# Kernel optimization log

Hardware: AMD Instinct MI355X
Metric: run time of the kernel (lower is better)

Reference implementation:

```python
import jax, jax.numpy as jnp
import numpy as np
from jax import lax

NUM_GROUPS = 16
POOL_KS = 2
CLAMP_MIN = 0.0
CLAMP_MAX = 1.0
EPS = 1e-5


def setup_inputs() -> dict:
    key = jax.random.key(0)
    k1, k2, k3, k4, k5 = jax.random.split(key, 5)
    B, Cin, H, W = 32, 64, 128, 128
    Cout, K = 128, 3
    x = jax.random.normal(k1, (B, Cin, H, W), dtype=jnp.float32)
    fan_in = Cin * K * K
    bound = 1.0 / np.sqrt(fan_in)
    conv_w = jax.random.uniform(k2, (Cout, Cin, K, K), jnp.float32, -bound, bound)
    conv_b = jax.random.uniform(k3, (Cout,), jnp.float32, -bound, bound)
    gn_w = jnp.ones((Cout,), jnp.float32)
    gn_b = jnp.zeros((Cout,), jnp.float32)
    scale = jnp.ones((Cout, 1, 1), jnp.float32)
    return {"x": x, "conv_w": conv_w, "conv_b": conv_b,
            "gn_w": gn_w, "gn_b": gn_b, "scale": scale}


def reference(x, conv_w, conv_b, gn_w, gn_b, scale):
    # Conv2d, stride=1, padding=0  -> (B, Cout, Ho, Wo)
    y = lax.conv_general_dilated(
        x, conv_w, window_strides=(1, 1), padding="VALID",
        dimension_numbers=("NCHW", "OIHW", "NCHW"))
    y = y + conv_b[None, :, None, None]
    B, C, H, W = y.shape
    G = NUM_GROUPS
    # GroupNorm (biased variance, as in torch)
    yg = y.reshape(B, G, C // G, H, W)
    mean = jnp.mean(yg, axis=(2, 3, 4), keepdims=True)
    var = jnp.mean(jnp.square(yg), axis=(2, 3, 4), keepdims=True) - jnp.square(mean)
    yn = (yg - mean) * lax.rsqrt(var + EPS)
    yn = yn.reshape(B, C, H, W) * gn_w[None, :, None, None] + gn_b[None, :, None, None]
    # per-channel scale
    yn = yn * scale[None, :, :, :]
    # MaxPool2d(kernel=POOL_KS, stride=POOL_KS), VALID
    pooled = lax.reduce_window(
        yn, -jnp.inf, lax.max,
        window_dimensions=(1, 1, POOL_KS, POOL_KS),
        window_strides=(1, 1, POOL_KS, POOL_KS),
        padding="VALID")
    return jnp.clip(pooled, CLAMP_MIN, CLAMP_MAX)
```

## Files before the change

kernel.cpp:

```cpp
#include <hip/hip_runtime.h>
#include <stdint.h>
#include <stddef.h>

#define HIN 128
#define WIN 128
#define CINC 64
#define COUTC 128
#define HO 126
#define WO 126
#define HP 63
#define WP 63
#define NB 32
#define NG 16

typedef __bf16 bf16x8 __attribute__((ext_vector_type(8)));
typedef float f32x16 __attribute__((ext_vector_type(16)));

#define AS1U(p) ((const __attribute__((address_space(1))) unsigned int*)(p))
#define AS3U(p) ((__attribute__((address_space(3))) unsigned int*)(p))

__device__ __forceinline__ unsigned int f2bf(float f) {
  unsigned int u = __float_as_uint(f);
  return (u + 0x7fffu + ((u >> 16) & 1u)) >> 16;
}

__global__ __launch_bounds__(256) void wtrans_k(const float* __restrict__ w,
                                                unsigned short* __restrict__ wt2) {
  int i = blockIdx.x * 256 + threadIdx.x;
  if (i >= 73728) return;
  int j = i & 7;
  int co = (i >> 3) & 127;
  int th = i >> 10;
  int half = th & 1, ks = (th >> 1) & 3, tap = th >> 3;
  int kh = tap / 3, kw = tap - 3 * kh;
  int cin = ks * 16 + half * 8 + j;
  float v = w[((co * CINC + cin) * 3 + kh) * 3 + kw];
  wt2[i] = (unsigned short)f2bf(v);
}

__global__ __launch_bounds__(256, 2) void conv_k(const float* __restrict__ x,
                                                 const unsigned short* __restrict__ wt2,
                                                 const float* __restrict__ conv_b,
                                                 float* __restrict__ out,
                                                 float* __restrict__ stats) {
  __shared__ __align__(16) unsigned int x_lds[18 * 18 * 32];
  __shared__ __align__(16) unsigned int aux_lds[8448];

  int t = threadIdx.x;
  int lane = t & 63, wave = t >> 6;
  int tw = blockIdx.x & 7, th = blockIdx.x >> 3;
  int b = blockIdx.y;
  int oh0 = th * 16, ow0 = tw * 16;

  const unsigned int* wg = (const unsigned int*)wt2;

#pragma unroll
  for (int j = 0; j < 4; ++j) {
    int dof = j * 1024 + wave * 256;
    __builtin_amdgcn_global_load_lds(AS1U(wg + dof + lane * 4), AS3U(&aux_lds[dof]),
                                     16, 0, 0);
  }

  const float* xb = x + (size_t)b * CINC * HIN * WIN;
  for (int i = t; i < 2880; i += 256) {
    int c4 = i % 5;
    int j = i / 5;
    int p = j & 31;
    int r = j >> 5;
    int gr = oh0 + r;
    int gc0 = ow0 + c4 * 4;
    float4 v0 = make_float4(0.f, 0.f, 0.f, 0.f);
    float4 v1 = v0;
    if (gr < HIN && gc0 < WIN) {
      const float* base = xb + ((size_t)(2 * p) * HIN + gr) * WIN + gc0;
      v0 = *(const float4*)base;
      v1 = *(const float4*)(base + HIN * WIN);
    }
    float e0[4] = {v0.x, v0.y, v0.z, v0.w};
    float e1[4] = {v1.x, v1.y, v1.z, v1.w};
#pragma unroll
    for (int cc = 0; cc < 4; ++cc) {
      int c = c4 * 4 + cc;
      if (c < 18) {
        unsigned int d = f2bf(e0[cc]) | (f2bf(e1[cc]) << 16);
        x_lds[(r * 18 + c) * 32 + (p ^ ((c & 7) << 2))] = d;
      }
    }
  }
  __syncthreads();

  int half = lane >> 5, m = lane & 31;
  f32x16 acc[2][4];
#pragma unroll
  for (int nt = 0; nt < 4; ++nt) {
    float bias = conv_b[nt * 32 + m];
#pragma unroll
    for (int mt = 0; mt < 2; ++mt)
#pragma unroll
      for (int r = 0; r < 16; ++r) acc[mt][nt][r] = bias;
  }

  int prb = wave * 4 + (m >> 4);
  int pcc = m & 15;

#pragma unroll
  for (int tap = 0; tap < 9; ++tap) {
    const int buf = tap & 1;
    if (tap < 8) {
#pragma unroll
      for (int j = 0; j < 4; ++j) {
        int dof = j * 1024 + wave * 256;
        __builtin_amdgcn_global_load_lds(
            AS1U(wg + (tap + 1) * 4096 + dof + lane * 4),
            AS3U(&aux_lds[(buf ^ 1) * 4096 + dof]), 16, 0, 0);
      }
    }
    const int kh = tap / 3, kw = tap - 3 * (tap / 3);
    int c = pcc + kw;
    int swz = (c & 7) << 2;
#pragma unroll
    for (int ks = 0; ks < 4; ++ks) {
      int ab = c * 32 + ((ks * 8 + half * 4) ^ swz);
      bf16x8 afr[2];
#pragma unroll
      for (int mt = 0; mt < 2; ++mt)
        afr[mt] = __builtin_bit_cast(
            bf16x8, *(const uint4*)&x_lds[(prb + mt * 2 + kh) * (18 * 32) + ab]);
      int wbase = buf * 4096 + ks * 1024 + half * 512 + m * 4;
#pragma unroll
      for (int nt = 0; nt < 4; ++nt) {
        bf16x8 bfr = __builtin_bit_cast(bf16x8, *(const uint4*)&aux_lds[wbase + nt * 128]);
#pragma unroll
        for (int mt = 0; mt < 2; ++mt)
          acc[mt][nt] = __builtin_amdgcn_mfma_f32_32x32x16_bf16(afr[mt], bfr,
                                                                acc[mt][nt], 0, 0, 0);
      }
    }
    __syncthreads();
  }

  float s[4] = {0.f, 0.f, 0.f, 0.f}, qs[4] = {0.f, 0.f, 0.f, 0.f};
#pragma unroll
  for (int nt = 0; nt < 4; ++nt) {
#pragma unroll
    for (int mt = 0; mt < 2; ++mt) {
#pragma unroll
      for (int reg = 0; reg < 16; ++reg) {
        int c16 = (reg & 3) + 4 * half + 8 * ((reg >> 2) & 1);
        int r8 = wave * 4 + mt * 2 + (reg >> 3);
        if ((oh0 + r8) < HO && (ow0 + c16) < WO) {
          float v = acc[mt][nt][reg];
          s[nt] += v;
          qs[nt] += v * v;
        }
      }
    }
  }
#pragma unroll
  for (int nt = 0; nt < 4; ++nt) {
    float sv = s[nt], qv = qs[nt];
    sv += __shfl_xor(sv, 32);
    qv += __shfl_xor(qv, 32);
    sv += __shfl_down(sv, 4, 8);
    qv += __shfl_down(qv, 4, 8);
    sv += __shfl_down(sv, 2, 8);
    qv += __shfl_down(qv, 2, 8);
    sv += __shfl_down(sv, 1, 8);
    qv += __shfl_down(qv, 1, 8);
    if (half == 0 && (m & 7) == 0) {
      int g = nt * 4 + (m >> 3);
      atomicAdd(&stats[(b * NG + g) * 2 + 0], sv);
      atomicAdd(&stats[(b * NG + g) * 2 + 1], qv);
    }
  }

#pragma unroll
  for (int nt = 0; nt < 4; ++nt) {
    int co = nt * 32 + m;
#pragma unroll
    for (int mt = 0; mt < 2; ++mt) {
      int oh2l = wave * 2 + mt;
#pragma unroll
      for (int i = 0; i < 4; ++i) {
        int r0 = 2 * i;
        int ow2l = (i & 1) + 2 * half + 4 * (i >> 1);
        float mx = fmaxf(fmaxf(acc[mt][nt][r0], acc[mt][nt][r0 + 1]),
                         fmaxf(acc[mt][nt][r0 + 8], acc[mt][nt][r0 + 9]));
        aux_lds[co * 66 + oh2l * 8 + ow2l] = __float_as_uint(mx);
      }
    }
  }
  __syncthreads();

#pragma unroll
  for (int i = 0; i < 4; ++i) {
    int row = t * 4 + i;
    int co = row >> 3, oh2l = row & 7;
    int oh2 = th * 8 + oh2l;
    if (oh2 < HP) {
      const uint2* src = (const uint2*)&aux_lds[co * 66 + oh2l * 8];
      uint2 d0 = src[0], d1 = src[1], d2 = src[2], d3 = src[3];
      unsigned int v[8] = {d0.x, d0.y, d1.x, d1.y, d2.x, d2.y, d3.x, d3.y};
      float* ob = out + ((size_t)(b * COUTC + co) * HP + oh2) * WP + tw * 8;
      int n = (tw == 7) ? 7 : 8;
#pragma unroll
      for (int e = 0; e < 8; ++e)
        if (e < n) ob[e] = __uint_as_float(v[e]);
    }
  }
}

__global__ __launch_bounds__(256) void fin_k(float* __restrict__ out,
                                             const float* __restrict__ stats,
                                             const float* __restrict__ gn_w,
                                             const float* __restrict__ gn_b,
                                             const float* __restrict__ scale) {
  const int total4 = NB * COUTC * HP * WP / 4;
  const float inv_cnt = 1.0f / (8.0f * HO * WO);
  int stride = gridDim.x * 256;
  for (int i4 = blockIdx.x * 256 + threadIdx.x; i4 < total4; i4 += stride) {
    float4 v = ((const float4*)out)[i4];
    float r[4] = {v.x, v.y, v.z, v.w};
    int idx0 = i4 * 4;
#pragma unroll
    for (int e = 0; e < 4; ++e) {
      int idx = idx0 + e;
      int bc = idx / (HP * WP);
      int c = bc & 127, b = bc >> 7;
      int g = c >> 3;
      float su = stats[(b * NG + g) * 2 + 0];
      float sq = stats[(b * NG + g) * 2 + 1];
      float mean = su * inv_cnt;
      float var = fmaxf(sq * inv_cnt - mean * mean, 0.f);
      float rstd = rsqrtf(var + 1e-5f);
      float A = rstd * gn_w[c] * scale[c];
      float B = (gn_b[c] - mean * rstd * gn_w[c]) * scale[c];
      r[e] = fminf(fmaxf(fmaf(r[e], A, B), 0.0f), 1.0f);
    }
    ((float4*)out)[i4] = make_float4(r[0], r[1], r[2], r[3]);
  }
}

extern "C" void kernel_launch(void* const* d_in, const int* in_sizes, int n_in,
                              void* d_out, int out_size, void* d_ws, size_t ws_size,
                              hipStream_t stream) {
  const float* x      = (const float*)d_in[0];
  const float* conv_w = (const float*)d_in[1];
  const float* conv_b = (const float*)d_in[2];
  const float* gn_w   = (const float*)d_in[3];
  const float* gn_b   = (const float*)d_in[4];
  const float* scale  = (const float*)d_in[5];
  float* out = (float*)d_out;

  float* stats        = (float*)d_ws;
  unsigned short* wt2 = (unsigned short*)((char*)d_ws + 4096);

  hipMemsetAsync(d_ws, 0, 4096, stream);
  wtrans_k<<<288, 256, 0, stream>>>(conv_w, wt2);

  conv_k<<<dim3(64, NB), 256, 0, stream>>>(x, wt2, conv_b, out, stats);

  fin_k<<<4096, 256, 0, stream>>>(out, stats, gn_w, gn_b, scale);
}
```

Before: 369.9 us.

## Load conv weights into registers, drop weight LDS, reorganize finalize per channel plane

The conv kernel no longer stages weights in LDS through global_load_lds. Each lane loads its B fragments straight from global memory into two register banks (wA/wB) that alternate across the nine taps, with the next tap's weights prefetched while the current tap's MFMAs run. Dropping the 33 KB aux buffer lets the pooled epilogue reuse x_lds, and the launch bound is raised to 3 blocks per CU. The finalize kernel now runs one block per (batch, channel) plane, computing the group-norm coefficients once instead of per element. The cost is 128 extra VGPRs for weight fragments, which may cause spills under the tighter launch bound, and duplicated global weight reads across waves.

```diff
diff --git a/kernel.cpp b/kernel.cpp
--- a/kernel.cpp
+++ b/kernel.cpp
@@ -15,9 +15,6 @@
 
 typedef __bf16 bf16x8 __attribute__((ext_vector_type(8)));
 typedef float f32x16 __attribute__((ext_vector_type(16)));
-
-#define AS1U(p) ((const __attribute__((address_space(1))) unsigned int*)(p))
-#define AS3U(p) ((__attribute__((address_space(3))) unsigned int*)(p))
 
 __device__ __forceinline__ unsigned int f2bf(float f) {
   unsigned int u = __float_as_uint(f);
@@ -38,28 +35,25 @@
   wt2[i] = (unsigned short)f2bf(v);
 }
 
-__global__ __launch_bounds__(256, 2) void conv_k(const float* __restrict__ x,
+__global__ __launch_bounds__(256, 3) void conv_k(const float* __restrict__ x,
                                                  const unsigned short* __restrict__ wt2,
                                                  const float* __restrict__ conv_b,
                                                  float* __restrict__ out,
                                                  float* __restrict__ stats) {
   __shared__ __align__(16) unsigned int x_lds[18 * 18 * 32];
-  __shared__ __align__(16) unsigned int aux_lds[8448];
 
   int t = threadIdx.x;
   int lane = t & 63, wave = t >> 6;
   int tw = blockIdx.x & 7, th = blockIdx.x >> 3;
   int b = blockIdx.y;
   int oh0 = th * 16, ow0 = tw * 16;
-
-  const unsigned int* wg = (const unsigned int*)wt2;
-
-#pragma unroll
-  for (int j = 0; j < 4; ++j) {
-    int dof = j * 1024 + wave * 256;
-    __builtin_amdgcn_global_load_lds(AS1U(wg + dof + lane * 4), AS3U(&aux_lds[dof]),
-                                     16, 0, 0);
-  }
+  int half = lane >> 5, m = lane & 31;
+
+  const uint4* wg4 = (const uint4*)wt2;
+  uint4 wA[16], wB[16];
+#pragma unroll
+  for (int i = 0; i < 16; ++i)
+    wA[i] = wg4[(i >> 2) * 256 + half * 128 + (i & 3) * 32 + m];
 
   const float* xb = x + (size_t)b * CINC * HIN * WIN;
   for (int i = t; i < 2880; i += 256) {
@@ -89,7 +83,6 @@
   }
   __syncthreads();
 
-  int half = lane >> 5, m = lane & 31;
   f32x16 acc[2][4];
 #pragma unroll
   for (int nt = 0; nt < 4; ++nt) {
@@ -103,41 +96,46 @@
   int prb = wave * 4 + (m >> 4);
   int pcc = m & 15;
 
-#pragma unroll
-  for (int tap = 0; tap < 9; ++tap) {
-    const int buf = tap & 1;
-    if (tap < 8) {
-#pragma unroll
-      for (int j = 0; j < 4; ++j) {
-        int dof = j * 1024 + wave * 256;
-        __builtin_amdgcn_global_load_lds(
-            AS1U(wg + (tap + 1) * 4096 + dof + lane * 4),
-            AS3U(&aux_lds[(buf ^ 1) * 4096 + dof]), 16, 0, 0);
-      }
-    }
-    const int kh = tap / 3, kw = tap - 3 * (tap / 3);
-    int c = pcc + kw;
-    int swz = (c & 7) << 2;
-#pragma unroll
-    for (int ks = 0; ks < 4; ++ks) {
-      int ab = c * 32 + ((ks * 8 + half * 4) ^ swz);
-      bf16x8 afr[2];
-#pragma unroll
-      for (int mt = 0; mt < 2; ++mt)
-        afr[mt] = __builtin_bit_cast(
-            bf16x8, *(const uint4*)&x_lds[(prb + mt * 2 + kh) * (18 * 32) + ab]);
-      int wbase = buf * 4096 + ks * 1024 + half * 512 + m * 4;
-#pragma unroll
-      for (int nt = 0; nt < 4; ++nt) {
-        bf16x8 bfr = __builtin_bit_cast(bf16x8, *(const uint4*)&aux_lds[wbase + nt * 128]);
-#pragma unroll
-        for (int mt = 0; mt < 2; ++mt)
-          acc[mt][nt] = __builtin_amdgcn_mfma_f32_32x32x16_bf16(afr[mt], bfr,
-                                                                acc[mt][nt], 0, 0, 0);
-      }
-    }
-    __syncthreads();
-  }
+#define CONV_TAP(tap, cur, nxt)                                                \
+  {                                                                            \
+    if ((tap) < 8) {                                                           \
+      _Pragma("unroll")                                                        \
+      for (int i = 0; i < 16; ++i)                                             \
+        nxt[i] = wg4[((tap) + 1) * 1024 + (i >> 2) * 256 + half * 128 +        \
+                     (i & 3) * 32 + m];                                        \
+    }                                                                          \
+    const int kh = (tap) / 3, kw = (tap) - 3 * ((tap) / 3);                    \
+    int c = pcc + kw;                                                          \
+    int swz = (c & 7) << 2;                                                    \
+    _Pragma("unroll")                                                          \
+    for (int ks = 0; ks < 4; ++ks) {                                           \
+      int ab = c * 32 + ((ks * 8 + half * 4) ^ swz);                           \
+      bf16x8 afr[2];                                                           \
+      _Pragma("unroll")                                                        \
+      for (int mt = 0; mt < 2; ++mt)                                           \
+        afr[mt] = __builtin_bit_cast(                                          \
+            bf16x8, *(const uint4*)&x_lds[(prb + mt * 2 + kh) * 576 + ab]);    \
+      _Pragma("unroll")                                                        \
+      for (int nt = 0; nt < 4; ++nt) {                                         \
+        bf16x8 bfr = __builtin_bit_cast(bf16x8, cur[ks * 4 + nt]);             \
+        _Pragma("unroll")                                                      \
+        for (int mt = 0; mt < 2; ++mt)                                         \
+          acc[mt][nt] = __builtin_amdgcn_mfma_f32_32x32x16_bf16(               \
+              afr[mt], bfr, acc[mt][nt], 0, 0, 0);                             \
+      }                                                                        \
+    }                                                                          \
+  }
+
+  CONV_TAP(0, wA, wB)
+  CONV_TAP(1, wB, wA)
+  CONV_TAP(2, wA, wB)
+  CONV_TAP(3, wB, wA)
+  CONV_TAP(4, wA, wB)
+  CONV_TAP(5, wB, wA)
+  CONV_TAP(6, wA, wB)
+  CONV_TAP(7, wB, wA)
+  CONV_TAP(8, wA, wB)
+#undef CONV_TAP
 
   float s[4] = {0.f, 0.f, 0.f, 0.f}, qs[4] = {0.f, 0.f, 0.f, 0.f};
 #pragma unroll
@@ -174,6 +172,8 @@
     }
   }
 
+  __syncthreads();
+
 #pragma unroll
   for (int nt = 0; nt < 4; ++nt) {
     int co = nt * 32 + m;
@@ -186,7 +186,7 @@
         int ow2l = (i & 1) + 2 * half + 4 * (i >> 1);
         float mx = fmaxf(fmaxf(acc[mt][nt][r0], acc[mt][nt][r0 + 1]),
                          fmaxf(acc[mt][nt][r0 + 8], acc[mt][nt][r0 + 9]));
-        aux_lds[co * 66 + oh2l * 8 + ow2l] = __float_as_uint(mx);
+        x_lds[co * 66 + oh2l * 8 + ow2l] = __float_as_uint(mx);
       }
     }
   }
@@ -198,7 +198,7 @@
     int co = row >> 3, oh2l = row & 7;
     int oh2 = th * 8 + oh2l;
     if (oh2 < HP) {
-      const uint2* src = (const uint2*)&aux_lds[co * 66 + oh2l * 8];
+      const uint2* src = (const uint2*)&x_lds[co * 66 + oh2l * 8];
       uint2 d0 = src[0], d1 = src[1], d2 = src[2], d3 = src[3];
       unsigned int v[8] = {d0.x, d0.y, d1.x, d1.y, d2.x, d2.y, d3.x, d3.y};
       float* ob = out + ((size_t)(b * COUTC + co) * HP + oh2) * WP + tw * 8;
@@ -215,30 +215,37 @@
                                              const float* __restrict__ gn_w,
                                              const float* __restrict__ gn_b,
                                              const float* __restrict__ scale) {
-  const int total4 = NB * COUTC * HP * WP / 4;
+  const int plane = HP * WP;
   const float inv_cnt = 1.0f / (8.0f * HO * WO);
-  int stride = gridDim.x * 256;
-  for (int i4 = blockIdx.x * 256 + threadIdx.x; i4 < total4; i4 += stride) {
-    float4 v = ((const float4*)out)[i4];
-    float r[4] = {v.x, v.y, v.z, v.w};
-    int idx0 = i4 * 4;
-#pragma unroll
-    for (int e = 0; e < 4; ++e) {
-      int idx = idx0 + e;
-      int bc = idx / (HP * WP);
-      int c = bc & 127, b = bc >> 7;
-      int g = c >> 3;
-      float su = stats[(b * NG + g) * 2 + 0];
-      float sq = stats[(b * NG + g) * 2 + 1];
-      float mean = su * inv_cnt;
-      float var = fmaxf(sq * inv_cnt - mean * mean, 0.f);
-      float rstd = rsqrtf(var + 1e-5f);
-      float A = rstd * gn_w[c] * scale[c];
-      float B = (gn_b[c] - mean * rstd * gn_w[c]) * scale[c];
-      r[e] = fminf(fmaxf(fmaf(r[e], A, B), 0.0f), 1.0f);
-    }
-    ((float4*)out)[i4] = make_float4(r[0], r[1], r[2], r[3]);
-  }
+  int bc = blockIdx.x;
+  int c = bc & 127, b = bc >> 7;
+  int g = c >> 3;
+  float su = stats[(b * NG + g) * 2 + 0];
+  float sq = stats[(b * NG + g) * 2 + 1];
+  float mean = su * inv_cnt;
+  float var = fmaxf(sq * inv_cnt - mean * mean, 0.f);
+  float rstd = rsqrtf(var + 1e-5f);
+  float gw = gn_w[c], sc = scale[c];
+  float A = rstd * gw * sc;
+  float Bo = (gn_b[c] - mean * rstd * gw) * sc;
+
+  float* p = out + (size_t)bc * plane;
+  int t = threadIdx.x;
+  int head = (4 - (bc & 3)) & 3;
+  if (t < head) p[t] = fminf(fmaxf(fmaf(p[t], A, Bo), 0.0f), 1.0f);
+  int n4 = (plane - head) >> 2;
+  float4* p4 = (float4*)(p + head);
+  for (int i = t; i < n4; i += 256) {
+    float4 v = p4[i];
+    v.x = fminf(fmaxf(fmaf(v.x, A, Bo), 0.0f), 1.0f);
+    v.y = fminf(fmaxf(fmaf(v.y, A, Bo), 0.0f), 1.0f);
+    v.z = fminf(fmaxf(fmaf(v.z, A, Bo), 0.0f), 1.0f);
+    v.w = fminf(fmaxf(fmaf(v.w, A, Bo), 0.0f), 1.0f);
+    p4[i] = v;
+  }
+  int done = head + (n4 << 2);
+  int tail = plane - done;
+  if (t < tail) p[done + t] = fminf(fmaxf(fmaf(p[done + t], A, Bo), 0.0f), 1.0f);
 }
 
 extern "C" void kernel_launch(void* const* d_in, const int* in_sizes, int n_in,
@@ -260,5 +267,5 @@
 
   conv_k<<<dim3(64, NB), 256, 0, stream>>>(x, wt2, conv_b, out, stats);
 
-  fin_k<<<4096, 256, 0, stream>>>(out, stats, gn_w, gn_b, scale);
-}
+  fin_k<<<NB * COUTC, 256, 0, stream>>>(out, stats, gn_w, gn_b, scale);
+}
```

Result: slower. 506.3 us (+36.9%).
